# Optimization experiments

Hardware: AMD Instinct MI355X
Metric: run time of the kernel (lower is better)

Reference implementation:

```python
import jax, jax.numpy as jnp
import numpy as np

# 8 trilerp corners in (x, y, z) component order, matching the original's
# [floor/ceil] enumeration: fff, ffc, fcf, fcc, cff, cfc, ccf, ccc.
CORNERS = np.array([[0, 0, 0], [0, 0, 1], [0, 1, 0], [0, 1, 1],
                    [1, 0, 0], [1, 0, 1], [1, 1, 0], [1, 1, 1]], dtype=np.int32)

N = 32768          # number of points
NUM_KERNELS = 4    # submodels
GRID = 16          # voxel grid size
C_IN = 64          # input_channels
C_OUT = 64         # features


def setup_inputs() -> dict:
    key = jax.random.key(0)
    k1, k2, k3, k4, k5 = jax.random.split(key, 5)
    param_idxs = jax.random.randint(k1, (N, 1), 0, NUM_KERNELS, dtype=jnp.int32)
    pos = jax.random.uniform(k2, (N, 3), dtype=jnp.float32)
    xs = jax.random.normal(k3, (N, C_IN), dtype=jnp.float32)
    # he_uniform over fan_in = input_channels
    limit = np.sqrt(6.0 / C_IN).astype(np.float32)
    kernels = jax.random.uniform(
        k4, (NUM_KERNELS, GRID, GRID, GRID, C_IN, C_OUT),
        dtype=jnp.float32, minval=-limit, maxval=limit)
    biases = jnp.zeros((NUM_KERNELS, GRID, GRID, GRID, C_OUT), dtype=jnp.float32)
    return {"param_idxs": param_idxs, "pos": pos, "xs": xs,
            "kernels": kernels, "biases": biases}


def reference(param_idxs, pos, xs, kernels, biases):
    """Trilinearly-interpolated per-point dense layer.

    Equivalent to building kernel = sum_c w_c * K_c and computing x @ kernel + bias;
    by linearity we accumulate w_c * (x @ K_c + b_c) directly, avoiding the
    materialized per-point interpolated kernel.
    """
    grid = kernels.shape[1]
    pidx = param_idxs.reshape(-1)            # (N,)
    loc = pos * grid - 0.5                    # (N, 3)
    floored = jnp.floor(loc)
    ceil_w = loc - floored                    # trilerp weights toward ceil
    floor_w = 1.0 - ceil_w
    out = jnp.zeros((pos.shape[0], kernels.shape[-1]), dtype=xs.dtype)
    for corner in CORNERS:                    # fixed 8-iteration loop
        idx = jnp.clip((floored + corner).astype(jnp.int32), 0, grid - 1)  # (N,3)
        w = jnp.prod(jnp.where(corner[None, :] == 1, ceil_w, floor_w), axis=-1)  # (N,)
        # Original indexes kernels[pidx, z, y, x] with z=idx[:,2], y=idx[:,1], x=idx[:,0]
        gk = kernels[pidx, idx[:, 2], idx[:, 1], idx[:, 0]]  # (N, C_in, C_out)
        gb = biases[pidx, idx[:, 2], idx[:, 1], idx[:, 0]]   # (N, C_out)
        out = out + w[:, None] * (jnp.einsum('nc,ncf->nf', xs, gk) + gb)
    return out
```

## Files before the change

kernel.cpp:

```cpp
#include <hip/hip_runtime.h>
#include <math.h>

#define NPTS   32768
#define NK     4
#define GRIDN  16
#define CIN    64
#define COUT   64
#define NCELLS (NK*GRIDN*GRIDN*GRIDN)
#define CAP    128

typedef __attribute__((ext_vector_type(8))) short  short8;
typedef __attribute__((ext_vector_type(4))) float  f32x4;

static __device__ inline unsigned short f2bf(float f) {
    unsigned int u = __builtin_bit_cast(unsigned int, f);
    unsigned int r = u + 0x7fff + ((u >> 16) & 1);
    return (unsigned short)(r >> 16);
}

__global__ void k_scatter(const int* __restrict__ pidx, const float* __restrict__ pos,
                          int* __restrict__ cnt, int2* __restrict__ ent,
                          int n, int cap) {
    int t = blockIdx.x * blockDim.x + threadIdx.x;
    int p = t >> 3;
    if (p >= n) return;
    int c  = t & 7;
    int pk = pidx[p];
    float lx = pos[3*p+0]*16.f - 0.5f;
    float ly = pos[3*p+1]*16.f - 0.5f;
    float lz = pos[3*p+2]*16.f - 0.5f;
    float flx = floorf(lx), fly = floorf(ly), flz = floorf(lz);
    float tx = lx - flx, ty = ly - fly, tz = lz - flz;
    int fx = (int)flx, fy = (int)fly, fz = (int)flz;
    int c0 = c & 1, c1 = (c >> 1) & 1, c2 = (c >> 2) & 1;
    int ix = min(max(fx + c0, 0), GRIDN-1);
    int iy = min(max(fy + c1, 0), GRIDN-1);
    int iz = min(max(fz + c2, 0), GRIDN-1);
    float w = (c0 ? tx : 1.f - tx) * (c1 ? ty : 1.f - ty) * (c2 ? tz : 1.f - tz);
    int cell = ((pk*GRIDN + iz)*GRIDN + iy)*GRIDN + ix;
    int e = atomicAdd(&cnt[cell], 1);
    if (e < cap) ent[(size_t)cell * cap + e] = make_int2(p, __float_as_int(w));
}

__global__ __launch_bounds__(256)
void k_main(const float* __restrict__ xs, const float* __restrict__ kernels,
            const float* __restrict__ biases, const int* __restrict__ cnt,
            const int2* __restrict__ ent, float* __restrict__ out, int cap) {
    int tid  = threadIdx.x;
    int wv   = tid >> 6;
    int l    = tid & 63;
    int q    = l >> 4;
    int m    = l & 15;
    int cell = blockIdx.x * 4 + wv;

    int count = min(cnt[cell], cap);
    if (count == 0) return;

    const float* Kg = kernels + (size_t)cell * (CIN * COUT);
    short8 Bf[4][2];
#pragma unroll
    for (int c = 0; c < 4; ++c)
#pragma unroll
        for (int s = 0; s < 2; ++s)
#pragma unroll
            for (int j = 0; j < 8; ++j)
                Bf[c][s][j] = (short)f2bf(Kg[(s*32 + q*8 + j)*COUT + c*16 + m]);

    float bias_c[4];
#pragma unroll
    for (int c = 0; c < 4; ++c)
        bias_c[c] = biases[(size_t)cell * COUT + c*16 + m];

    const int2* eb = ent + (size_t)cell * cap;
    int nb = (count + 15) >> 4;
    for (int b = 0; b < nb; ++b) {
        int r0 = b << 4;
        int2 em = (r0 + m < count) ? eb[r0 + m] : make_int2(0, 0);
        int apid = em.x;

        short8 af[2];
#pragma unroll
        for (int s = 0; s < 2; ++s) {
            const float4 x0 = *(const float4*)&xs[(size_t)apid*CIN + s*32 + q*8 + 0];
            const float4 x1 = *(const float4*)&xs[(size_t)apid*CIN + s*32 + q*8 + 4];
            af[s][0] = (short)f2bf(x0.x); af[s][1] = (short)f2bf(x0.y);
            af[s][2] = (short)f2bf(x0.z); af[s][3] = (short)f2bf(x0.w);
            af[s][4] = (short)f2bf(x1.x); af[s][5] = (short)f2bf(x1.y);
            af[s][6] = (short)f2bf(x1.z); af[s][7] = (short)f2bf(x1.w);
        }

        f32x4 acc[4];
#pragma unroll
        for (int c = 0; c < 4; ++c) acc[c] = (f32x4){0.f, 0.f, 0.f, 0.f};
#pragma unroll
        for (int s = 0; s < 2; ++s)
#pragma unroll
            for (int c = 0; c < 4; ++c)
                acc[c] = __builtin_amdgcn_mfma_f32_16x16x32_bf16(af[s], Bf[c][s], acc[c], 0, 0, 0);

#pragma unroll
        for (int reg = 0; reg < 4; ++reg) {
            int   r     = q*4 + reg;
            int   pid_r = __shfl(em.x, r);
            float w_r   = __shfl(__int_as_float(em.y), r);
            if (w_r != 0.f) {
                float* orow = out + (size_t)pid_r * COUT + m;
#pragma unroll
                for (int c = 0; c < 4; ++c)
                    unsafeAtomicAdd(&orow[c*16], w_r * (acc[c][reg] + bias_c[c]));
            }
        }
    }
}

extern "C" void kernel_launch(void* const* d_in, const int* in_sizes, int n_in,
                              void* d_out, int out_size, void* d_ws, size_t ws_size,
                              hipStream_t stream) {
    const int*   pidx    = (const int*)  d_in[0];
    const float* pos     = (const float*)d_in[1];
    const float* xs      = (const float*)d_in[2];
    const float* kernels = (const float*)d_in[3];
    const float* biases  = (const float*)d_in[4];
    float*       out     = (float*)d_out;
    int n = in_sizes[0];

    int*  cnt = (int*)d_ws;
    int2* ent = (int2*)((char*)d_ws + (size_t)NCELLS * sizeof(int));

    int cap = CAP;
    size_t avail = (ws_size > (size_t)NCELLS * sizeof(int))
                 ? (ws_size - (size_t)NCELLS * sizeof(int)) / (sizeof(int2) * NCELLS)
                 : 0;
    if ((size_t)cap > avail) cap = (int)avail;

    hipMemsetAsync(cnt, 0, NCELLS * sizeof(int), stream);
    hipMemsetAsync(d_out, 0, (size_t)out_size * sizeof(float), stream);

    int eblocks = (n * 8 + 255) / 256;
    k_scatter<<<eblocks, 256, 0, stream>>>(pidx, pos, cnt, ent, n, cap);
    k_main  <<<NCELLS/4, 256, 0, stream>>>(xs, kernels, biases, cnt, ent, out, cap);
}
```

Baseline: 396.3 us.

## Replace output atomics with per-corner staging buffer plus reduction, pre-convert xs to bf16

The scatter kernel now also converts xs to bf16 once, so the main kernel loads short8 fragments directly instead of loading fp32 and converting per cell. Each entry encodes its corner index. The main kernel writes weighted results into an 8-slot staging buffer indexed by corner instead of doing atomic adds into the output, and a new reduce kernel sums the 8 slots. The entry list for the next batch is also prefetched. In exchange it adds about 128MB of staging writes and reads plus an extra launch. It also drops the workspace-size check on cap and the early exit for empty cells, and staging slots are left unwritten if a cell overflows cap.

```diff
diff --git a/kernel.cpp b/kernel.cpp
--- a/kernel.cpp
+++ b/kernel.cpp
@@ -19,9 +19,23 @@
 }
 
 __global__ void k_scatter(const int* __restrict__ pidx, const float* __restrict__ pos,
+                          const float* __restrict__ xs, unsigned short* __restrict__ xb,
                           int* __restrict__ cnt, int2* __restrict__ ent,
                           int n, int cap) {
     int t = blockIdx.x * blockDim.x + threadIdx.x;
+
+    {
+        int o = t * 8;
+        if (o + 8 <= n * CIN) {
+            float4 a = *(const float4*)&xs[o + 0];
+            float4 b = *(const float4*)&xs[o + 4];
+            ushort4 lo = { f2bf(a.x), f2bf(a.y), f2bf(a.z), f2bf(a.w) };
+            ushort4 hi = { f2bf(b.x), f2bf(b.y), f2bf(b.z), f2bf(b.w) };
+            *(ushort4*)&xb[o + 0] = lo;
+            *(ushort4*)&xb[o + 4] = hi;
+        }
+    }
+
     int p = t >> 3;
     if (p >= n) return;
     int c  = t & 7;
@@ -39,13 +53,13 @@
     float w = (c0 ? tx : 1.f - tx) * (c1 ? ty : 1.f - ty) * (c2 ? tz : 1.f - tz);
     int cell = ((pk*GRIDN + iz)*GRIDN + iy)*GRIDN + ix;
     int e = atomicAdd(&cnt[cell], 1);
-    if (e < cap) ent[(size_t)cell * cap + e] = make_int2(p, __float_as_int(w));
+    if (e < cap) ent[(size_t)cell * cap + e] = make_int2(p | (c << 20), __float_as_int(w));
 }
 
 __global__ __launch_bounds__(256)
-void k_main(const float* __restrict__ xs, const float* __restrict__ kernels,
+void k_main(const unsigned short* __restrict__ xb, const float* __restrict__ kernels,
             const float* __restrict__ biases, const int* __restrict__ cnt,
-            const int2* __restrict__ ent, float* __restrict__ out, int cap) {
+            const int2* __restrict__ ent, float* __restrict__ stage, int cap) {
     int tid  = threadIdx.x;
     int wv   = tid >> 6;
     int l    = tid & 63;
@@ -54,7 +68,9 @@
     int cell = blockIdx.x * 4 + wv;
 
     int count = min(cnt[cell], cap);
-    if (count == 0) return;
+    const int2* eb = ent + (size_t)cell * cap;
+
+    int2 em = (m < count) ? eb[m] : make_int2(0, 0);
 
     const float* Kg = kernels + (size_t)cell * (CIN * COUT);
     short8 Bf[4][2];
@@ -71,23 +87,18 @@
     for (int c = 0; c < 4; ++c)
         bias_c[c] = biases[(size_t)cell * COUT + c*16 + m];
 
-    const int2* eb = ent + (size_t)cell * cap;
     int nb = (count + 15) >> 4;
     for (int b = 0; b < nb; ++b) {
         int r0 = b << 4;
-        int2 em = (r0 + m < count) ? eb[r0 + m] : make_int2(0, 0);
-        int apid = em.x;
+        int2 em_n = make_int2(0, 0);
+        if (b + 1 < nb && r0 + 16 + m < count) em_n = eb[r0 + 16 + m];
+
+        int apid = em.x & 0xFFFFF;
 
         short8 af[2];
 #pragma unroll
-        for (int s = 0; s < 2; ++s) {
-            const float4 x0 = *(const float4*)&xs[(size_t)apid*CIN + s*32 + q*8 + 0];
-            const float4 x1 = *(const float4*)&xs[(size_t)apid*CIN + s*32 + q*8 + 4];
-            af[s][0] = (short)f2bf(x0.x); af[s][1] = (short)f2bf(x0.y);
-            af[s][2] = (short)f2bf(x0.z); af[s][3] = (short)f2bf(x0.w);
-            af[s][4] = (short)f2bf(x1.x); af[s][5] = (short)f2bf(x1.y);
-            af[s][6] = (short)f2bf(x1.z); af[s][7] = (short)f2bf(x1.w);
-        }
+        for (int s = 0; s < 2; ++s)
+            af[s] = *(const short8*)&xb[(size_t)apid*CIN + s*32 + q*8];
 
         f32x4 acc[4];
 #pragma unroll
@@ -101,16 +112,34 @@
 #pragma unroll
         for (int reg = 0; reg < 4; ++reg) {
             int   r     = q*4 + reg;
-            int   pid_r = __shfl(em.x, r);
+            int   key_r = __shfl(em.x, r);
             float w_r   = __shfl(__int_as_float(em.y), r);
-            if (w_r != 0.f) {
-                float* orow = out + (size_t)pid_r * COUT + m;
+            if (r0 + r < count) {
+                int pid_r = key_r & 0xFFFFF;
+                int c_r   = key_r >> 20;
+                float* srow = stage + ((size_t)c_r * NPTS + pid_r) * COUT + m;
 #pragma unroll
                 for (int c = 0; c < 4; ++c)
-                    unsafeAtomicAdd(&orow[c*16], w_r * (acc[c][reg] + bias_c[c]));
+                    srow[c*16] = w_r * (acc[c][reg] + bias_c[c]);
             }
         }
+        em = em_n;
     }
+}
+
+__global__ __launch_bounds__(256)
+void k_reduce(const float* __restrict__ stage, float* __restrict__ out) {
+    int t  = blockIdx.x * blockDim.x + threadIdx.x;
+    int p  = t >> 4;
+    int c4 = (t & 15) << 2;
+    size_t off = (size_t)p * COUT + c4;
+    float4 s = *(const float4*)&stage[off];
+#pragma unroll
+    for (int c = 1; c < 8; ++c) {
+        float4 v = *(const float4*)&stage[(size_t)c * NPTS * COUT + off];
+        s.x += v.x; s.y += v.y; s.z += v.z; s.w += v.w;
+    }
+    *(float4*)&out[off] = s;
 }
 
 extern "C" void kernel_launch(void* const* d_in, const int* in_sizes, int n_in,
@@ -124,19 +153,18 @@
     float*       out     = (float*)d_out;
     int n = in_sizes[0];
 
-    int*  cnt = (int*)d_ws;
-    int2* ent = (int2*)((char*)d_ws + (size_t)NCELLS * sizeof(int));
+    char* w = (char*)d_ws;
+    int*            cnt   = (int*)w;                 w += (size_t)NCELLS * sizeof(int);
+    int2*           ent   = (int2*)w;                w += (size_t)NCELLS * CAP * sizeof(int2);
+    unsigned short* xb    = (unsigned short*)w;      w += (size_t)NPTS * CIN * sizeof(unsigned short);
+    float*          stage = (float*)w;
 
     int cap = CAP;
-    size_t avail = (ws_size > (size_t)NCELLS * sizeof(int))
-                 ? (ws_size - (size_t)NCELLS * sizeof(int)) / (sizeof(int2) * NCELLS)
-                 : 0;
-    if ((size_t)cap > avail) cap = (int)avail;
 
     hipMemsetAsync(cnt, 0, NCELLS * sizeof(int), stream);
-    hipMemsetAsync(d_out, 0, (size_t)out_size * sizeof(float), stream);
 
     int eblocks = (n * 8 + 255) / 256;
-    k_scatter<<<eblocks, 256, 0, stream>>>(pidx, pos, cnt, ent, n, cap);
-    k_main  <<<NCELLS/4, 256, 0, stream>>>(xs, kernels, biases, cnt, ent, out, cap);
+    k_scatter<<<eblocks, 256, 0, stream>>>(pidx, pos, xs, xb, cnt, ent, n, cap);
+    k_main  <<<NCELLS/4, 256, 0, stream>>>(xb, kernels, biases, cnt, ent, stage, cap);
+    k_reduce<<<(NPTS*16)/256, 256, 0, stream>>>(stage, out);
 }
```

After: 410.6 us. 3.6% more time.
